# Kernel tuning notes

Hardware: AMD Instinct MI355X
Metric: run time of the kernel (lower is better)

The kernel has to match this reference:

```python
import jax, jax.numpy as jnp
import numpy as np

N, E, F_IN, H, C = 40000, 640000, 128, 128, 32


def _xavier(k, shape):
    gain = np.sqrt(2.0)  # calculate_gain('relu')
    bound = gain * np.sqrt(6.0 / (shape[0] + shape[1]))
    return jax.random.uniform(k, shape, jnp.float32, -bound, bound)


def setup_inputs() -> dict:
    key = jax.random.key(0)
    ks = jax.random.split(key, 8)
    features = jax.random.normal(ks[0], (N, F_IN), jnp.float32)
    src = jax.random.randint(ks[1], (E,), 0, N)
    dst = jax.random.randint(ks[2], (E,), 0, N)
    weight = jax.random.uniform(ks[3], (E, 1), jnp.float32, minval=0.1, maxval=1.0)
    W1 = _xavier(ks[4], (H, F_IN)); b1 = jnp.zeros((H,), jnp.float32)
    W2 = _xavier(ks[5], (H, H));    b2 = jnp.zeros((H,), jnp.float32)
    Wo = _xavier(ks[6], (C, H));    bo = jnp.zeros((C,), jnp.float32)
    return dict(features=features, src=src, dst=dst, weight=weight,
                W1=W1, b1=b1, W2=W2, b2=b2, Wo=Wo, bo=bo)


def _aggregate(h, src, dst, w):
    # message: m = h[src] * w  (weighted gather-multiply)
    # reduce:  neigh = deg * sum(m) / ((deg+1) * sum(w)) + h / (deg+1)
    n = h.shape[0]
    m = h[src] * w                                            # [E, D]
    sum_m = jax.ops.segment_sum(m, dst, num_segments=n)       # [N, D]
    sum_w = jax.ops.segment_sum(w[:, 0], dst, num_segments=n) # [N]
    deg = jax.ops.segment_sum(jnp.ones((src.shape[0],), h.dtype), dst, num_segments=n)
    denom = (deg + 1.0) * jnp.where(sum_w == 0.0, 1.0, sum_w)
    neigh = deg[:, None] * sum_m / denom[:, None] + h / (deg[:, None] + 1.0)
    # nodes with no in-edges never get reduce_func applied -> neigh stays 0
    return jnp.where(deg[:, None] > 0.0, neigh, 0.0)


def reference(features, src, dst, weight, W1, b1, W2, b2, Wo, bo):
    h = features
    for W, b in ((W1, b1), (W2, b2)):
        neigh = _aggregate(h, src, dst, weight)
        h = jax.nn.relu(neigh @ W.T + b)  # NodeUpdate: fc_neigh + activation
    return h @ Wo.T + bo                  # final classifier linear
```

## Files before the change

kernel.cpp:

```cpp
#include <hip/hip_runtime.h>


#define D 128

__global__ void count_kernel(const int* __restrict__ dst, int* __restrict__ deg, int e) {
    int i = blockIdx.x * blockDim.x + threadIdx.x;
    if (i < e) atomicAdd(&deg[dst[i]], 1);
}

__global__ void scan_kernel(const int* __restrict__ deg, int* __restrict__ rowptr, int n) {
    __shared__ int part[1024];
    const int t = threadIdx.x;
    const int per = (n + 1023) / 1024;
    const int beg = t * per;
    const int end = min(n, beg + per);
    int s = 0;
    for (int i = beg; i < end; ++i) s += deg[i];
    part[t] = s;
    __syncthreads();
    for (int off = 1; off < 1024; off <<= 1) {
        int v = (t >= off) ? part[t - off] : 0;
        __syncthreads();
        part[t] += v;
        __syncthreads();
    }
    int base = part[t] - s;
    for (int i = beg; i < end; ++i) { rowptr[i] = base; base += deg[i]; }
    if (t == 1023) rowptr[n] = part[1023];
}

__global__ void scatter_kernel(const int* __restrict__ src, const int* __restrict__ dst,
                               const float* __restrict__ w, const int* __restrict__ rowptr,
                               int* __restrict__ cur, int* __restrict__ csrc,
                               float* __restrict__ cw, int e) {
    int i = blockIdx.x * blockDim.x + threadIdx.x;
    if (i < e) {
        int d = dst[i];
        int pos = rowptr[d] + atomicAdd(&cur[d], 1);
        csrc[pos] = src[i];
        cw[pos]   = w[i];
    }
}

__global__ __launch_bounds__(256) void agg_kernel(
        const float* __restrict__ h, const int* __restrict__ rowptr,
        const int* __restrict__ csrc, const float* __restrict__ cw,
        float* __restrict__ neigh, int n) {
    const int wid  = (blockIdx.x * blockDim.x + threadIdx.x) >> 6;
    const int lane = threadIdx.x & 63;
    if (wid >= n) return;
    const int beg = rowptr[wid], end = rowptr[wid + 1];
    float2 a0 = {0.f, 0.f}, a1 = {0.f, 0.f}, a2 = {0.f, 0.f}, a3 = {0.f, 0.f};
    float ws = 0.f;
    const int co = lane * 2;
    int e = beg;
    if ((e & 1) && e < end) {
        int s0 = csrc[e]; float w0 = cw[e];
        float2 v0 = *(const float2*)(h + (size_t)s0 * D + co);
        a0.x = fmaf(v0.x, w0, a0.x); a0.y = fmaf(v0.y, w0, a0.y);
        ws += w0; ++e;
    }
    for (; e + 3 < end; e += 4) {
        int2   s01 = *(const int2*)(csrc + e), s23 = *(const int2*)(csrc + e + 2);
        float2 w01 = *(const float2*)(cw + e), w23 = *(const float2*)(cw + e + 2);
        float2 v0 = *(const float2*)(h + (size_t)s01.x * D + co);
        float2 v1 = *(const float2*)(h + (size_t)s01.y * D + co);
        float2 v2 = *(const float2*)(h + (size_t)s23.x * D + co);
        float2 v3 = *(const float2*)(h + (size_t)s23.y * D + co);
        a0.x = fmaf(v0.x, w01.x, a0.x); a0.y = fmaf(v0.y, w01.x, a0.y);
        a1.x = fmaf(v1.x, w01.y, a1.x); a1.y = fmaf(v1.y, w01.y, a1.y);
        a2.x = fmaf(v2.x, w23.x, a2.x); a2.y = fmaf(v2.y, w23.x, a2.y);
        a3.x = fmaf(v3.x, w23.y, a3.x); a3.y = fmaf(v3.y, w23.y, a3.y);
        ws += (w01.x + w01.y) + (w23.x + w23.y);
    }
    for (; e < end; ++e) {
        int s0 = csrc[e]; float w0 = cw[e];
        float2 v0 = *(const float2*)(h + (size_t)s0 * D + co);
        a0.x = fmaf(v0.x, w0, a0.x); a0.y = fmaf(v0.y, w0, a0.y);
        ws += w0;
    }
    a0.x += a1.x + a2.x + a3.x;
    a0.y += a1.y + a2.y + a3.y;
    float2 o = {0.f, 0.f};
    if (end > beg) {
        const float deg  = (float)(end - beg);
        const float sw   = (ws == 0.f) ? 1.f : ws;
        const float invm = deg / ((deg + 1.f) * sw);
        const float invd = 1.f / (deg + 1.f);
        float2 hc = *(const float2*)(h + (size_t)wid * D + co);
        o.x = fmaf(a0.x, invm, hc.x * invd);
        o.y = fmaf(a0.y, invm, hc.y * invd);
    }
    *(float2*)(neigh + (size_t)wid * D + co) = o;
}

template <int OUT, int TM, bool RELU>
__global__ __launch_bounds__(256) void fc_kernel(
        const float* __restrict__ X, const float* __restrict__ W,
        const float* __restrict__ B, float* __restrict__ Y, int n) {
    constexpr int TNX = OUT / 4;
    constexpr int TY  = 256 / TNX;
    constexpr int NT  = TY * TM;
    __shared__ float sWt[D][OUT];
    __shared__ float sN[NT][D];
    const int t = threadIdx.x;
    for (int p = t; p < OUT * (D / 4); p += 256) {
        int j = p % OUT, k4 = (p / OUT) << 2;
        const float4 v = *(const float4*)(W + j * D + k4);
        sWt[k4 + 0][j] = v.x; sWt[k4 + 1][j] = v.y;
        sWt[k4 + 2][j] = v.z; sWt[k4 + 3][j] = v.w;
    }
    const int tx = t % TNX, ty = t / TNX;
    const float4 bv = *(const float4*)(B + tx * 4);
    const int ntiles = (n + NT - 1) / NT;
    for (int tile = blockIdx.x; tile < ntiles; tile += gridDim.x) {
        const int node0 = tile * NT;
        __syncthreads();
        for (int p = t; p < NT * (D / 4); p += 256) {
            int r = p >> 5, c = (p & 31) << 2;
            int nd = node0 + r;
            float4 v = make_float4(0.f, 0.f, 0.f, 0.f);
            if (nd < n) v = *(const float4*)(X + (size_t)nd * D + c);
            *(float4*)&sN[r][c] = v;
        }
        __syncthreads();
        float acc[TM][4];
        #pragma unroll
        for (int m = 0; m < TM; ++m)
            acc[m][0] = acc[m][1] = acc[m][2] = acc[m][3] = 0.f;
        #pragma unroll 2
        for (int k = 0; k < D; k += 4) {
            float4 xv[TM];
            #pragma unroll
            for (int m = 0; m < TM; ++m) xv[m] = *(const float4*)&sN[ty * TM + m][k];
            #pragma unroll
            for (int i = 0; i < 4; ++i) {
                const float4 wv = *(const float4*)&sWt[k + i][tx * 4];
                #pragma unroll
                for (int m = 0; m < TM; ++m) {
                    const float x = (i == 0) ? xv[m].x : (i == 1) ? xv[m].y
                                  : (i == 2) ? xv[m].z : xv[m].w;
                    acc[m][0] = fmaf(x, wv.x, acc[m][0]);
                    acc[m][1] = fmaf(x, wv.y, acc[m][1]);
                    acc[m][2] = fmaf(x, wv.z, acc[m][2]);
                    acc[m][3] = fmaf(x, wv.w, acc[m][3]);
                }
            }
        }
        #pragma unroll
        for (int m = 0; m < TM; ++m) {
            const int nd = node0 + ty * TM + m;
            if (nd < n) {
                float4 o;
                o.x = acc[m][0] + bv.x; o.y = acc[m][1] + bv.y;
                o.z = acc[m][2] + bv.z; o.w = acc[m][3] + bv.w;
                if (RELU) {
                    o.x = fmaxf(o.x, 0.f); o.y = fmaxf(o.y, 0.f);
                    o.z = fmaxf(o.z, 0.f); o.w = fmaxf(o.w, 0.f);
                }
                *(float4*)(Y + (size_t)nd * OUT + tx * 4) = o;
            }
        }
    }
}

extern "C" void kernel_launch(void* const* d_in, const int* in_sizes, int n_in,
                              void* d_out, int out_size, void* d_ws, size_t ws_size,
                              hipStream_t stream) {
    const float* feat = (const float*)d_in[0];
    const int*   src  = (const int*)d_in[1];
    const int*   dst  = (const int*)d_in[2];
    const float* w    = (const float*)d_in[3];
    const float* W1   = (const float*)d_in[4];
    const float* b1   = (const float*)d_in[5];
    const float* W2   = (const float*)d_in[6];
    const float* b2   = (const float*)d_in[7];
    const float* Wo   = (const float*)d_in[8];
    const float* bo   = (const float*)d_in[9];
    float* out = (float*)d_out;

    const int n = in_sizes[0] / D;
    const int e = in_sizes[1];

    char* ws = (char*)d_ws;
    size_t off = 0;
    auto carve = [&](size_t bytes) {
        char* p = ws + off;
        off = (off + bytes + 255) & ~(size_t)255;
        return p;
    };
    int*   deg    = (int*)carve((size_t)n * 4);
    int*   cur    = (int*)carve((size_t)n * 4);
    int*   rowptr = (int*)carve((size_t)(n + 1) * 4);
    int*   csrc   = (int*)carve((size_t)e * 4);
    float* cw     = (float*)carve((size_t)e * 4);
    float* neigh  = (float*)carve((size_t)n * D * 4);
    float* hbuf   = (float*)carve((size_t)n * D * 4);

    const int TB = 256;
    hipMemsetAsync(deg, 0, (size_t)((char*)(cur + n) - (char*)deg), stream);
    count_kernel<<<(e + TB - 1) / TB, TB, 0, stream>>>(dst, deg, e);
    scan_kernel<<<1, 1024, 0, stream>>>(deg, rowptr, n);
    scatter_kernel<<<(e + TB - 1) / TB, TB, 0, stream>>>(src, dst, w, rowptr, cur, csrc, cw, e);

    const int aggBlocks = (n + 3) / 4;
    const int fc128Grid = 512;
    const int fc32Grid  = (n + 63) / 64;

    agg_kernel<<<aggBlocks, TB, 0, stream>>>(feat, rowptr, csrc, cw, neigh, n);
    fc_kernel<128, 4, true><<<fc128Grid, TB, 0, stream>>>(neigh, W1, b1, hbuf, n);
    agg_kernel<<<aggBlocks, TB, 0, stream>>>(hbuf, rowptr, csrc, cw, neigh, n);
    fc_kernel<128, 4, true><<<fc128Grid, TB, 0, stream>>>(neigh, W2, b2, hbuf, n);
    fc_kernel<32, 2, false><<<fc32Grid, TB, 0, stream>>>(hbuf, Wo, bo, out, n);
}
```

Measured before the change: 373.5 us.

## Parallelize CSR prefix scan across blocks and split edges across half-waves in aggregation

Replaces the single-block serial-chunk scan with a three-kernel multi-block scan (block sums, a wave-level scan of the block sums, then per-block scan and write), so rowptr construction is no longer limited to one workgroup. The aggregation kernel now has each half of a 64-lane wave handle alternating edges with float4 loads and combines the halves with a cross-lane shuffle, doubling the gather width per instruction. This adds two extra kernel launches and a shuffle reduction. The block-sum scan handles at most 64 blocks, which is enough for n up to 65536 only.

```diff
diff --git a/kernel.cpp b/kernel.cpp
--- a/kernel.cpp
+++ b/kernel.cpp
@@ -8,25 +8,48 @@
     if (i < e) atomicAdd(&deg[dst[i]], 1);
 }
 
-__global__ void scan_kernel(const int* __restrict__ deg, int* __restrict__ rowptr, int n) {
+__global__ void scan_blocksum(const int* __restrict__ deg, int* __restrict__ bsum, int n) {
+    __shared__ int red[1024];
+    const int t = threadIdx.x;
+    const int i = blockIdx.x * 1024 + t;
+    red[t] = (i < n) ? deg[i] : 0;
+    __syncthreads();
+    for (int off = 512; off > 0; off >>= 1) {
+        if (t < off) red[t] += red[t + off];
+        __syncthreads();
+    }
+    if (t == 0) bsum[blockIdx.x] = red[0];
+}
+
+__global__ void scan_bsum(const int* __restrict__ bsum, int* __restrict__ bbase, int nb) {
+    const int l = threadIdx.x;
+    int s = (l < nb) ? bsum[l] : 0;
+    int v = s;
+    for (int off = 1; off < 64; off <<= 1) {
+        int u = __shfl_up(v, off, 64);
+        if (l >= off) v += u;
+    }
+    if (l < nb) bbase[l] = v - s;
+}
+
+__global__ void scan_write(const int* __restrict__ deg, const int* __restrict__ bbase,
+                           int* __restrict__ rowptr, int n) {
     __shared__ int part[1024];
     const int t = threadIdx.x;
-    const int per = (n + 1023) / 1024;
-    const int beg = t * per;
-    const int end = min(n, beg + per);
-    int s = 0;
-    for (int i = beg; i < end; ++i) s += deg[i];
-    part[t] = s;
+    const int i = blockIdx.x * 1024 + t;
+    const int v = (i < n) ? deg[i] : 0;
+    part[t] = v;
     __syncthreads();
     for (int off = 1; off < 1024; off <<= 1) {
-        int v = (t >= off) ? part[t - off] : 0;
-        __syncthreads();
-        part[t] += v;
-        __syncthreads();
-    }
-    int base = part[t] - s;
-    for (int i = beg; i < end; ++i) { rowptr[i] = base; base += deg[i]; }
-    if (t == 1023) rowptr[n] = part[1023];
+        int u = (t >= off) ? part[t - off] : 0;
+        __syncthreads();
+        part[t] += u;
+        __syncthreads();
+    }
+    const int incl = part[t];
+    const int base = bbase[blockIdx.x];
+    if (i < n) rowptr[i] = base + incl - v;
+    if (i == n - 1) rowptr[n] = base + incl;
 }
 
 __global__ void scatter_kernel(const int* __restrict__ src, const int* __restrict__ dst,
@@ -49,49 +72,68 @@
     const int wid  = (blockIdx.x * blockDim.x + threadIdx.x) >> 6;
     const int lane = threadIdx.x & 63;
     if (wid >= n) return;
+    const int half = lane >> 5;
+    const int q4   = (lane & 31) << 2;
     const int beg = rowptr[wid], end = rowptr[wid + 1];
-    float2 a0 = {0.f, 0.f}, a1 = {0.f, 0.f}, a2 = {0.f, 0.f}, a3 = {0.f, 0.f};
+    float4 aA = {0.f, 0.f, 0.f, 0.f}, aB = {0.f, 0.f, 0.f, 0.f};
     float ws = 0.f;
-    const int co = lane * 2;
     int e = beg;
     if ((e & 1) && e < end) {
-        int s0 = csrc[e]; float w0 = cw[e];
-        float2 v0 = *(const float2*)(h + (size_t)s0 * D + co);
-        a0.x = fmaf(v0.x, w0, a0.x); a0.y = fmaf(v0.y, w0, a0.y);
+        int s0 = csrc[e]; float w0 = half ? 0.f : cw[e];
+        const float4 v = *(const float4*)(h + (size_t)s0 * D + q4);
+        aA.x = fmaf(v.x, w0, aA.x); aA.y = fmaf(v.y, w0, aA.y);
+        aA.z = fmaf(v.z, w0, aA.z); aA.w = fmaf(v.w, w0, aA.w);
         ws += w0; ++e;
     }
     for (; e + 3 < end; e += 4) {
-        int2   s01 = *(const int2*)(csrc + e), s23 = *(const int2*)(csrc + e + 2);
-        float2 w01 = *(const float2*)(cw + e), w23 = *(const float2*)(cw + e + 2);
-        float2 v0 = *(const float2*)(h + (size_t)s01.x * D + co);
-        float2 v1 = *(const float2*)(h + (size_t)s01.y * D + co);
-        float2 v2 = *(const float2*)(h + (size_t)s23.x * D + co);
-        float2 v3 = *(const float2*)(h + (size_t)s23.y * D + co);
-        a0.x = fmaf(v0.x, w01.x, a0.x); a0.y = fmaf(v0.y, w01.x, a0.y);
-        a1.x = fmaf(v1.x, w01.y, a1.x); a1.y = fmaf(v1.y, w01.y, a1.y);
-        a2.x = fmaf(v2.x, w23.x, a2.x); a2.y = fmaf(v2.y, w23.x, a2.y);
-        a3.x = fmaf(v3.x, w23.y, a3.x); a3.y = fmaf(v3.y, w23.y, a3.y);
-        ws += (w01.x + w01.y) + (w23.x + w23.y);
-    }
-    for (; e < end; ++e) {
-        int s0 = csrc[e]; float w0 = cw[e];
-        float2 v0 = *(const float2*)(h + (size_t)s0 * D + co);
-        a0.x = fmaf(v0.x, w0, a0.x); a0.y = fmaf(v0.y, w0, a0.y);
+        int2   sA = *(const int2*)(csrc + e), sB = *(const int2*)(csrc + e + 2);
+        float2 wA = *(const float2*)(cw + e), wB = *(const float2*)(cw + e + 2);
+        const int   iA = half ? sA.y : sA.x,  iB = half ? sB.y : sB.x;
+        const float fA = half ? wA.y : wA.x,  fB = half ? wB.y : wB.x;
+        const float4 vA = *(const float4*)(h + (size_t)iA * D + q4);
+        const float4 vB = *(const float4*)(h + (size_t)iB * D + q4);
+        aA.x = fmaf(vA.x, fA, aA.x); aA.y = fmaf(vA.y, fA, aA.y);
+        aA.z = fmaf(vA.z, fA, aA.z); aA.w = fmaf(vA.w, fA, aA.w);
+        aB.x = fmaf(vB.x, fB, aB.x); aB.y = fmaf(vB.y, fB, aB.y);
+        aB.z = fmaf(vB.z, fB, aB.z); aB.w = fmaf(vB.w, fB, aB.w);
+        ws += fA + fB;
+    }
+    if (e + 1 < end) {
+        int2   sA = *(const int2*)(csrc + e);
+        float2 wA = *(const float2*)(cw + e);
+        const int   iA = half ? sA.y : sA.x;
+        const float fA = half ? wA.y : wA.x;
+        const float4 vA = *(const float4*)(h + (size_t)iA * D + q4);
+        aA.x = fmaf(vA.x, fA, aA.x); aA.y = fmaf(vA.y, fA, aA.y);
+        aA.z = fmaf(vA.z, fA, aA.z); aA.w = fmaf(vA.w, fA, aA.w);
+        ws += fA; e += 2;
+    }
+    if (e < end) {
+        int s0 = csrc[e]; float w0 = half ? 0.f : cw[e];
+        const float4 v = *(const float4*)(h + (size_t)s0 * D + q4);
+        aA.x = fmaf(v.x, w0, aA.x); aA.y = fmaf(v.y, w0, aA.y);
+        aA.z = fmaf(v.z, w0, aA.z); aA.w = fmaf(v.w, w0, aA.w);
         ws += w0;
     }
-    a0.x += a1.x + a2.x + a3.x;
-    a0.y += a1.y + a2.y + a3.y;
-    float2 o = {0.f, 0.f};
-    if (end > beg) {
-        const float deg  = (float)(end - beg);
-        const float sw   = (ws == 0.f) ? 1.f : ws;
-        const float invm = deg / ((deg + 1.f) * sw);
-        const float invd = 1.f / (deg + 1.f);
-        float2 hc = *(const float2*)(h + (size_t)wid * D + co);
-        o.x = fmaf(a0.x, invm, hc.x * invd);
-        o.y = fmaf(a0.y, invm, hc.y * invd);
-    }
-    *(float2*)(neigh + (size_t)wid * D + co) = o;
+    aA.x += aB.x; aA.y += aB.y; aA.z += aB.z; aA.w += aB.w;
+    aA.x += __shfl_xor(aA.x, 32); aA.y += __shfl_xor(aA.y, 32);
+    aA.z += __shfl_xor(aA.z, 32); aA.w += __shfl_xor(aA.w, 32);
+    ws   += __shfl_xor(ws, 32);
+    if (!half) {
+        float4 o = {0.f, 0.f, 0.f, 0.f};
+        if (end > beg) {
+            const float deg  = (float)(end - beg);
+            const float sw   = (ws == 0.f) ? 1.f : ws;
+            const float invm = deg / ((deg + 1.f) * sw);
+            const float invd = 1.f / (deg + 1.f);
+            const float4 hc = *(const float4*)(h + (size_t)wid * D + q4);
+            o.x = fmaf(aA.x, invm, hc.x * invd);
+            o.y = fmaf(aA.y, invm, hc.y * invd);
+            o.z = fmaf(aA.z, invm, hc.z * invd);
+            o.w = fmaf(aA.w, invm, hc.w * invd);
+        }
+        *(float4*)(neigh + (size_t)wid * D + q4) = o;
+    }
 }
 
 template <int OUT, int TM, bool RELU>
@@ -196,11 +238,16 @@
     float* cw     = (float*)carve((size_t)e * 4);
     float* neigh  = (float*)carve((size_t)n * D * 4);
     float* hbuf   = (float*)carve((size_t)n * D * 4);
+    const int nScanBlk = (n + 1023) / 1024;
+    int* bsum  = (int*)carve((size_t)nScanBlk * 4);
+    int* bbase = (int*)carve((size_t)nScanBlk * 4);
 
     const int TB = 256;
     hipMemsetAsync(deg, 0, (size_t)((char*)(cur + n) - (char*)deg), stream);
     count_kernel<<<(e + TB - 1) / TB, TB, 0, stream>>>(dst, deg, e);
-    scan_kernel<<<1, 1024, 0, stream>>>(deg, rowptr, n);
+    scan_blocksum<<<nScanBlk, 1024, 0, stream>>>(deg, bsum, n);
+    scan_bsum<<<1, 64, 0, stream>>>(bsum, bbase, nScanBlk);
+    scan_write<<<nScanBlk, 1024, 0, stream>>>(deg, bbase, rowptr, n);
     scatter_kernel<<<(e + TB - 1) / TB, TB, 0, stream>>>(src, dst, w, rowptr, cur, csrc, cw, e);
 
     const int aggBlocks = (n + 3) / 4;
```

Result: faster. 315.1 us (-15.6%).
